# Kernel tuning notes

Measured on AMD Instinct MI355X. Metric: run time of the kernel, lower is better.

## Reference

```python
import jax, jax.numpy as jnp
import numpy as np

N_DOMAINS = 8
LN_EPS = 1e-5


def setup_inputs() -> dict:
    key = jax.random.key(0)
    ks = jax.random.split(key, 4)
    N, D_IN, D_HID, D_OUT = 32768, 256, 1024, 256
    x = jax.random.normal(ks[0], (N, D_IN), dtype=jnp.float32)
    domain_types = jax.random.randint(ks[1], (N,), 0, N_DOMAINS, dtype=jnp.int32)
    # Per-domain MLP parameters (8 independent experts)
    W1 = jax.random.normal(ks[2], (N_DOMAINS, D_IN, D_HID), dtype=jnp.float32) * (1.0 / np.sqrt(D_IN))
    b1 = jnp.zeros((N_DOMAINS, D_HID), dtype=jnp.float32)
    gamma = jnp.ones((N_DOMAINS, D_HID), dtype=jnp.float32)
    beta = jnp.zeros((N_DOMAINS, D_HID), dtype=jnp.float32)
    W2 = jax.random.normal(ks[3], (N_DOMAINS, D_HID, D_OUT), dtype=jnp.float32) * (1.0 / np.sqrt(D_HID))
    b2 = jnp.zeros((N_DOMAINS, D_OUT), dtype=jnp.float32)
    return {"x": x, "domain_types": domain_types, "W1": W1, "b1": b1,
            "gamma": gamma, "beta": beta, "W2": W2, "b2": b2}


def _expert_mlp(x, W1d, b1d, gd, bd, W2d, b2d):
    # Linear -> LayerNorm -> ReLU -> (Dropout: identity at eval) -> Linear
    h = x @ W1d + b1d                       # [N, hid]
    mu = jnp.mean(h, axis=-1, keepdims=True)
    var = jnp.mean(jnp.square(h - mu), axis=-1, keepdims=True)
    h = (h - mu) * jax.lax.rsqrt(var + LN_EPS) * gd + bd
    h = jax.nn.relu(h)
    return h @ W2d + b2d                    # [N, out]


def reference(x, domain_types, W1, b1, gamma, beta, W2, b2):
    # output dim == x.shape[-1] (as in the torch code: zeros(batch, x.shape[-1]))
    out = jnp.zeros((x.shape[0], x.shape[-1]), dtype=x.dtype)
    for d in range(N_DOMAINS):  # small fixed expert loop (static MoE dispatch)
        y = _expert_mlp(x, W1[d], b1[d], gamma[d], beta[d], W2[d], b2[d])
        mask = (domain_types == d)[:, None]
        out = jnp.where(mask, y, out)
    return out
```

## Files before the change

kernel.cpp:

```cpp
#include <hip/hip_runtime.h>
#include <hip/hip_bf16.h>


#define ND 8
#define NROWS 32768
#define DIN 256
#define DHID 1024
#define DOUT 256
#define MPAD 33792
#define NTILES 264

typedef short short8 __attribute__((ext_vector_type(8)));
typedef float floatx4 __attribute__((ext_vector_type(4)));

__device__ __forceinline__ unsigned short f2bf(float f) {
    unsigned u = __builtin_bit_cast(unsigned, f);
    unsigned r = u + 0x7fff + ((u >> 16) & 1);
    return (unsigned short)(r >> 16);
}
__device__ __forceinline__ float bf2f(unsigned short h) {
    unsigned u = ((unsigned)h) << 16;
    return __builtin_bit_cast(float, u);
}

#define GLDS16(gp, lp) __builtin_amdgcn_global_load_lds( \
    (const __attribute__((address_space(1))) void*)(gp), \
    (__attribute__((address_space(3))) void*)(lp), 16, 0, 0)

__global__ void transpose_bf16(const float* __restrict__ in,
                               unsigned short* __restrict__ out,
                               int R, int C) {
    __shared__ float t[32][33];
    const int z = blockIdx.z;
    const int c0 = blockIdx.x * 32, r0 = blockIdx.y * 32;
    const int tx = threadIdx.x & 31, ty = threadIdx.x >> 5;
    const float* src = in + (size_t)z * R * C;
    unsigned short* dst = out + (size_t)z * R * C;
#pragma unroll
    for (int i = 0; i < 32; i += 8)
        t[ty + i][tx] = src[(size_t)(r0 + ty + i) * C + c0 + tx];
    __syncthreads();
#pragma unroll
    for (int i = 0; i < 32; i += 8)
        dst[(size_t)(c0 + ty + i) * R + r0 + tx] = f2bf(t[tx][ty + i]);
}

__global__ void zero_init(int* __restrict__ perm, int* __restrict__ rowdom,
                          int* __restrict__ cnt) {
    int i = blockIdx.x * 256 + threadIdx.x;
    if (i < MPAD) { perm[i] = -1; rowdom[i] = 0; }
    if (i < 16) cnt[i] = 0;
}

__global__ void histo(const int* __restrict__ dt, int* __restrict__ counts) {
    __shared__ int lc[ND];
    if (threadIdx.x < ND) lc[threadIdx.x] = 0;
    __syncthreads();
    int i = blockIdx.x * 256 + threadIdx.x;
    atomicAdd(&lc[dt[i]], 1);
    __syncthreads();
    if (threadIdx.x < ND) atomicAdd(&counts[threadIdx.x], lc[threadIdx.x]);
}

__global__ void make_meta(const int* __restrict__ counts, int* __restrict__ cursors,
                          int2* __restrict__ meta) {
    if (threadIdx.x == 0 && blockIdx.x == 0) {
        int off = 0, t = 0;
        for (int d = 0; d < ND; d++) {
            cursors[d] = off;
            int nt = (counts[d] + 127) >> 7;
            for (int i = 0; i < nt; i++) meta[t++] = make_int2(d, off + (i << 7));
            off += nt << 7;
        }
        for (; t < NTILES; t++) meta[t] = make_int2(-1, 0);
    }
}

__global__ __launch_bounds__(256)
void assign_pos(const int* __restrict__ dt, int* __restrict__ cursors,
                int* __restrict__ perm, int* __restrict__ rowdom,
                int* __restrict__ pos) {
    __shared__ int lcnt[ND];
    __shared__ int lbase[ND];
    const int tid = threadIdx.x;
    if (tid < ND) lcnt[tid] = 0;
    __syncthreads();
    const int r = blockIdx.x * 256 + tid;
    const int d = dt[r];
    const int myrank = atomicAdd(&lcnt[d], 1);
    __syncthreads();
    if (tid < ND && lcnt[tid] > 0)
        lbase[tid] = atomicAdd(&cursors[tid], lcnt[tid]);
    __syncthreads();
    const int p = lbase[d] + myrank;
    pos[r] = p;
    perm[p] = r;
    rowdom[p] = d;
}

__global__ __launch_bounds__(256)
void copy_rows(const float* __restrict__ x, const int* __restrict__ pos,
               unsigned short* __restrict__ xs) {
    const int tid = threadIdx.x;
    const int lane = tid & 63;
    const int r = blockIdx.x * 4 + (tid >> 6);
    const int p = pos[r];
    float4 v = ((const float4*)(x + (size_t)r * DIN))[lane];
    ushort4 o;
    o.x = f2bf(v.x); o.y = f2bf(v.y); o.z = f2bf(v.z); o.w = f2bf(v.w);
    ((ushort4*)(xs + (size_t)p * DIN))[lane] = o;
}

template <int K, bool SCATTER>
__global__ __launch_bounds__(256, 2)
void gemm_bt(const unsigned short* __restrict__ A,
             const unsigned short* __restrict__ Bt,
             const float* __restrict__ bias,
             const int2* __restrict__ meta,
             const int* __restrict__ perm,
             unsigned short* __restrict__ Cbf,
             float* __restrict__ Cf,
             const int Ntot) {
    const int2 md = meta[blockIdx.x];
    const int dom = md.x;
    if (dom < 0) return;
    const int m0 = md.y;
    const int n0 = blockIdx.y * 128;

    __shared__ unsigned short As[128 * 32];
    __shared__ unsigned short Bs[128 * 32];

    const int tid = threadIdx.x;
    const int lane = tid & 63;
    const int w = tid >> 6;
    const int wr = w >> 1, wc = w & 1;

    const unsigned short* Abase = A + (size_t)m0 * K;
    const unsigned short* Bbase = Bt + (size_t)dom * Ntot * K + (size_t)n0 * K;

    floatx4 acc[4][4];
#pragma unroll
    for (int i = 0; i < 4; i++)
#pragma unroll
        for (int j = 0; j < 4; j++) acc[i][j] = 0.f;

    for (int k0 = 0; k0 < K; k0 += 32) {
#pragma unroll
        for (int it = 0; it < 2; ++it) {
            const int c = w * 128 + it * 64 + lane;
            const int m = c >> 2, kc = c & 3;
            GLDS16(Abase + (size_t)m * K + k0 + kc * 8, &As[(w * 128 + it * 64) * 8]);
            GLDS16(Bbase + (size_t)m * K + k0 + kc * 8, &Bs[(w * 128 + it * 64) * 8]);
        }
        __syncthreads();

        short8 a[4], b[4];
        const int kk = (lane >> 4) * 8;
#pragma unroll
        for (int i = 0; i < 4; i++) {
            const int m = wr * 64 + i * 16 + (lane & 15);
            a[i] = *(const short8*)&As[m * 32 + kk];
            const int n = wc * 64 + i * 16 + (lane & 15);
            b[i] = *(const short8*)&Bs[n * 32 + kk];
        }
#pragma unroll
        for (int i = 0; i < 4; i++)
#pragma unroll
            for (int j = 0; j < 4; j++)
                acc[i][j] = __builtin_amdgcn_mfma_f32_16x16x32_bf16(a[i], b[j], acc[i][j], 0, 0, 0);
        __syncthreads();
    }

    const int quad = lane >> 4;
#pragma unroll
    for (int i = 0; i < 4; i++) {
        const int rowbase = m0 + wr * 64 + i * 16 + quad * 4;
        if (!SCATTER) {
#pragma unroll
            for (int j = 0; j < 4; j++) {
                const int col = n0 + wc * 64 + j * 16 + (lane & 15);
                const float bv = bias[dom * Ntot + col];
#pragma unroll
                for (int r = 0; r < 4; r++)
                    Cbf[(size_t)(rowbase + r) * Ntot + col] = f2bf(acc[i][j][r] + bv);
            }
        } else {
#pragma unroll
            for (int r = 0; r < 4; r++) {
                const int orig = perm[rowbase + r];
                if (orig < 0) continue;
#pragma unroll
                for (int j = 0; j < 4; j++) {
                    const int col = n0 + wc * 64 + j * 16 + (lane & 15);
                    Cf[(size_t)orig * Ntot + col] = acc[i][j][r] + bias[dom * Ntot + col];
                }
            }
        }
    }
}

__global__ __launch_bounds__(256)
void ln_relu(unsigned short* __restrict__ H, const float* __restrict__ gamma,
             const float* __restrict__ beta, const int* __restrict__ rowdom) {
    const int row = blockIdx.x;
    const int tid = threadIdx.x;
    const int dom = rowdom[row];
    unsigned short* hr = H + (size_t)row * DHID;
    ushort4 raw = ((const ushort4*)hr)[tid];
    float v0 = bf2f(raw.x), v1 = bf2f(raw.y), v2 = bf2f(raw.z), v3 = bf2f(raw.w);
    float s = v0 + v1 + v2 + v3;
    float s2 = v0 * v0 + v1 * v1 + v2 * v2 + v3 * v3;
#pragma unroll
    for (int o = 32; o; o >>= 1) {
        s += __shfl_xor(s, o, 64);
        s2 += __shfl_xor(s2, o, 64);
    }
    __shared__ float red[8];
    const int w = tid >> 6;
    if ((tid & 63) == 0) { red[w] = s; red[4 + w] = s2; }
    __syncthreads();
    s = red[0] + red[1] + red[2] + red[3];
    s2 = red[4] + red[5] + red[6] + red[7];
    const float inv = 1.0f / 1024.0f;
    const float mu = s * inv;
    const float var = fmaxf(s2 * inv - mu * mu, 0.f);
    const float rstd = rsqrtf(var + 1e-5f);
    const float* g = gamma + dom * DHID + tid * 4;
    const float* b = beta + dom * DHID + tid * 4;
    ushort4 o4;
    o4.x = f2bf(fmaxf((v0 - mu) * rstd * g[0] + b[0], 0.f));
    o4.y = f2bf(fmaxf((v1 - mu) * rstd * g[1] + b[1], 0.f));
    o4.z = f2bf(fmaxf((v2 - mu) * rstd * g[2] + b[2], 0.f));
    o4.w = f2bf(fmaxf((v3 - mu) * rstd * g[3] + b[3], 0.f));
    ((ushort4*)hr)[tid] = o4;
}

extern "C" void kernel_launch(void* const* d_in, const int* in_sizes, int n_in,
                              void* d_out, int out_size, void* d_ws, size_t ws_size,
                              hipStream_t stream) {
    const float* x = (const float*)d_in[0];
    const int* dt = (const int*)d_in[1];
    const float* W1 = (const float*)d_in[2];
    const float* b1 = (const float*)d_in[3];
    const float* gamma = (const float*)d_in[4];
    const float* beta = (const float*)d_in[5];
    const float* W2 = (const float*)d_in[6];
    const float* b2 = (const float*)d_in[7];
    float* out = (float*)d_out;

    char* ws = (char*)d_ws;
    size_t off = 0;
    auto take = [&](size_t nbytes) -> char* {
        char* p = ws + off;
        off = (off + nbytes + 255) & ~(size_t)255;
        return p;
    };
    unsigned short* W1T = (unsigned short*)take((size_t)ND * DHID * DIN * 2);
    unsigned short* W2T = (unsigned short*)take((size_t)ND * DOUT * DHID * 2);
    unsigned short* XS  = (unsigned short*)take((size_t)MPAD * DIN * 2);
    unsigned short* H   = (unsigned short*)take((size_t)MPAD * DHID * 2);
    int* PERM   = (int*)take(MPAD * 4);
    int* ROWDOM = (int*)take(MPAD * 4);
    int* POS    = (int*)take(NROWS * 4);
    int* CNT    = (int*)take(64);
    int2* META  = (int2*)take(NTILES * 8);
    (void)ws_size; (void)n_in; (void)in_sizes; (void)out_size;

    int* COUNTS = CNT;
    int* CURSORS = CNT + 8;

    transpose_bf16<<<dim3(DHID / 32, DIN / 32, ND), 256, 0, stream>>>(W1, W1T, DIN, DHID);
    transpose_bf16<<<dim3(DOUT / 32, DHID / 32, ND), 256, 0, stream>>>(W2, W2T, DHID, DOUT);
    zero_init<<<(MPAD + 255) / 256, 256, 0, stream>>>(PERM, ROWDOM, CNT);
    histo<<<NROWS / 256, 256, 0, stream>>>(dt, COUNTS);
    make_meta<<<1, 1, 0, stream>>>(COUNTS, CURSORS, META);
    assign_pos<<<NROWS / 256, 256, 0, stream>>>(dt, CURSORS, PERM, ROWDOM, POS);
    copy_rows<<<NROWS / 4, 256, 0, stream>>>(x, POS, XS);
    gemm_bt<DIN, false><<<dim3(NTILES, DHID / 128), 256, 0, stream>>>(
        XS, W1T, b1, META, nullptr, H, nullptr, DHID);
    ln_relu<<<MPAD, 256, 0, stream>>>(H, gamma, beta, ROWDOM);
    gemm_bt<DHID, true><<<dim3(NTILES, DOUT / 128), 256, 0, stream>>>(
        H, W2T, b2, META, PERM, nullptr, out, DOUT);
}
```

Baseline: 227.6 us.

## Fuse gather, both expert GEMMs and LayerNorm into one per-tile kernel

Replaces the copy_rows, first GEMM, ln_relu and second GEMM kernels with a single fused kernel. Each 512-thread block owns a 64-row tile and gathers x rows through perm into swizzled LDS. It computes the full 1024-wide hidden layer in registers, does the LayerNorm reduction across waves, writes the bf16 activations back to LDS, and runs the second GEMM with a scatter store. This removes the round trips of XS and H through global memory and several launches. In exchange it uses 128KB+ of LDS per block, which limits occupancy, reads weights directly from global without LDS staging, and makes make_meta parallel.

```diff
diff --git a/kernel.cpp b/kernel.cpp
--- a/kernel.cpp
+++ b/kernel.cpp
@@ -7,8 +7,9 @@
 #define DIN 256
 #define DHID 1024
 #define DOUT 256
-#define MPAD 33792
-#define NTILES 264
+#define RPT 64
+#define MPAD64 33280
+#define NT64 520
 
 typedef short short8 __attribute__((ext_vector_type(8)));
 typedef float floatx4 __attribute__((ext_vector_type(4)));
@@ -18,14 +19,6 @@
     unsigned r = u + 0x7fff + ((u >> 16) & 1);
     return (unsigned short)(r >> 16);
 }
-__device__ __forceinline__ float bf2f(unsigned short h) {
-    unsigned u = ((unsigned)h) << 16;
-    return __builtin_bit_cast(float, u);
-}
-
-#define GLDS16(gp, lp) __builtin_amdgcn_global_load_lds( \
-    (const __attribute__((address_space(1))) void*)(gp), \
-    (__attribute__((address_space(3))) void*)(lp), 16, 0, 0)
 
 __global__ void transpose_bf16(const float* __restrict__ in,
                                unsigned short* __restrict__ out,
@@ -45,10 +38,9 @@
         dst[(size_t)(c0 + ty + i) * R + r0 + tx] = f2bf(t[tx][ty + i]);
 }
 
-__global__ void zero_init(int* __restrict__ perm, int* __restrict__ rowdom,
-                          int* __restrict__ cnt) {
+__global__ void zero_init(int* __restrict__ perm, int* __restrict__ cnt) {
     int i = blockIdx.x * 256 + threadIdx.x;
-    if (i < MPAD) { perm[i] = -1; rowdom[i] = 0; }
+    if (i < MPAD64) perm[i] = -1;
     if (i < 16) cnt[i] = 0;
 }
 
@@ -64,22 +56,32 @@
 
 __global__ void make_meta(const int* __restrict__ counts, int* __restrict__ cursors,
                           int2* __restrict__ meta) {
-    if (threadIdx.x == 0 && blockIdx.x == 0) {
-        int off = 0, t = 0;
+    __shared__ int base[ND], ntc[ND];
+    const int t = threadIdx.x;
+    if (t == 0) {
+        int off = 0;
         for (int d = 0; d < ND; d++) {
+            base[d] = off;
+            ntc[d] = (counts[d] + 63) >> 6;
             cursors[d] = off;
-            int nt = (counts[d] + 127) >> 7;
-            for (int i = 0; i < nt; i++) meta[t++] = make_int2(d, off + (i << 7));
-            off += nt << 7;
-        }
-        for (; t < NTILES; t++) meta[t] = make_int2(-1, 0);
+            off += ntc[d] << 6;
+        }
+    }
+    __syncthreads();
+    for (int i = t; i < NT64; i += 64) {
+        int2 m = make_int2(-1, 0);
+#pragma unroll
+        for (int d = 0; d < ND; d++) {
+            const int ti = i - (base[d] >> 6);
+            if (ti >= 0 && ti < ntc[d]) m = make_int2(d, base[d] + (ti << 6));
+        }
+        meta[i] = m;
     }
 }
 
 __global__ __launch_bounds__(256)
 void assign_pos(const int* __restrict__ dt, int* __restrict__ cursors,
-                int* __restrict__ perm, int* __restrict__ rowdom,
-                int* __restrict__ pos) {
+                int* __restrict__ perm) {
     __shared__ int lcnt[ND];
     __shared__ int lbase[ND];
     const int tid = threadIdx.x;
@@ -92,147 +94,242 @@
     if (tid < ND && lcnt[tid] > 0)
         lbase[tid] = atomicAdd(&cursors[tid], lcnt[tid]);
     __syncthreads();
-    const int p = lbase[d] + myrank;
-    pos[r] = p;
-    perm[p] = r;
-    rowdom[p] = d;
-}
-
-__global__ __launch_bounds__(256)
-void copy_rows(const float* __restrict__ x, const int* __restrict__ pos,
-               unsigned short* __restrict__ xs) {
-    const int tid = threadIdx.x;
-    const int lane = tid & 63;
-    const int r = blockIdx.x * 4 + (tid >> 6);
-    const int p = pos[r];
-    float4 v = ((const float4*)(x + (size_t)r * DIN))[lane];
-    ushort4 o;
-    o.x = f2bf(v.x); o.y = f2bf(v.y); o.z = f2bf(v.z); o.w = f2bf(v.w);
-    ((ushort4*)(xs + (size_t)p * DIN))[lane] = o;
-}
-
-template <int K, bool SCATTER>
-__global__ __launch_bounds__(256, 2)
-void gemm_bt(const unsigned short* __restrict__ A,
-             const unsigned short* __restrict__ Bt,
-             const float* __restrict__ bias,
-             const int2* __restrict__ meta,
-             const int* __restrict__ perm,
-             unsigned short* __restrict__ Cbf,
-             float* __restrict__ Cf,
-             const int Ntot) {
-    const int2 md = meta[blockIdx.x];
+    perm[lbase[d] + myrank] = r;
+}
+
+__global__ __launch_bounds__(512, 2)
+void fused_mlp(const float* __restrict__ x,
+               const unsigned short* __restrict__ W1T,
+               const float* __restrict__ b1,
+               const float* __restrict__ gamma,
+               const float* __restrict__ beta,
+               const unsigned short* __restrict__ W2T,
+               const float* __restrict__ b2,
+               const int2* __restrict__ meta,
+               const int* __restrict__ perm,
+               float* __restrict__ out) {
+    const int bid = (int)blockIdx.x;
+    const int swz = (bid & 7) * (NT64 >> 3) + (bid >> 3);
+    const int2 md = meta[swz];
     const int dom = md.x;
     if (dom < 0) return;
     const int m0 = md.y;
-    const int n0 = blockIdx.y * 128;
-
-    __shared__ unsigned short As[128 * 32];
-    __shared__ unsigned short Bs[128 * 32];
+
+    __shared__ unsigned short Hs[RPT * DHID];
+    __shared__ float red[1024];
+    unsigned short* Axs = Hs;
 
     const int tid = threadIdx.x;
     const int lane = tid & 63;
     const int w = tid >> 6;
-    const int wr = w >> 1, wc = w & 1;
-
-    const unsigned short* Abase = A + (size_t)m0 * K;
-    const unsigned short* Bbase = Bt + (size_t)dom * Ntot * K + (size_t)n0 * K;
-
-    floatx4 acc[4][4];
-#pragma unroll
-    for (int i = 0; i < 4; i++)
-#pragma unroll
-        for (int j = 0; j < 4; j++) acc[i][j] = 0.f;
-
-    for (int k0 = 0; k0 < K; k0 += 32) {
-#pragma unroll
-        for (int it = 0; it < 2; ++it) {
-            const int c = w * 128 + it * 64 + lane;
-            const int m = c >> 2, kc = c & 3;
-            GLDS16(Abase + (size_t)m * K + k0 + kc * 8, &As[(w * 128 + it * 64) * 8]);
-            GLDS16(Bbase + (size_t)m * K + k0 + kc * 8, &Bs[(w * 128 + it * 64) * 8]);
-        }
-        __syncthreads();
-
-        short8 a[4], b[4];
-        const int kk = (lane >> 4) * 8;
-#pragma unroll
-        for (int i = 0; i < 4; i++) {
-            const int m = wr * 64 + i * 16 + (lane & 15);
-            a[i] = *(const short8*)&As[m * 32 + kk];
-            const int n = wc * 64 + i * 16 + (lane & 15);
-            b[i] = *(const short8*)&Bs[n * 32 + kk];
-        }
-#pragma unroll
-        for (int i = 0; i < 4; i++)
-#pragma unroll
-            for (int j = 0; j < 4; j++)
-                acc[i][j] = __builtin_amdgcn_mfma_f32_16x16x32_bf16(a[i], b[j], acc[i][j], 0, 0, 0);
-        __syncthreads();
-    }
-
-    const int quad = lane >> 4;
-#pragma unroll
-    for (int i = 0; i < 4; i++) {
-        const int rowbase = m0 + wr * 64 + i * 16 + quad * 4;
-        if (!SCATTER) {
-#pragma unroll
-            for (int j = 0; j < 4; j++) {
-                const int col = n0 + wc * 64 + j * 16 + (lane & 15);
-                const float bv = bias[dom * Ntot + col];
-#pragma unroll
-                for (int r = 0; r < 4; r++)
-                    Cbf[(size_t)(rowbase + r) * Ntot + col] = f2bf(acc[i][j][r] + bv);
+    const int l15 = lane & 15;
+    const int q = lane >> 4;
+
+    {
+        const int row = tid >> 3;
+        const int c8 = tid & 7;
+        const int orig = perm[m0 + row];
+        const int sw = (row & 7) << 3;
+        if (orig >= 0) {
+            const float4* src = (const float4*)(x + (size_t)orig * DIN);
+#pragma unroll
+            for (int it = 0; it < 8; ++it) {
+                const int c = it * 8 + c8;
+                const float4 v = src[c];
+                ushort4 o;
+                o.x = f2bf(v.x); o.y = f2bf(v.y); o.z = f2bf(v.z); o.w = f2bf(v.w);
+                *(ushort4*)&Axs[(row * DIN + c * 4) ^ sw] = o;
             }
         } else {
-#pragma unroll
-            for (int r = 0; r < 4; r++) {
-                const int orig = perm[rowbase + r];
-                if (orig < 0) continue;
-#pragma unroll
-                for (int j = 0; j < 4; j++) {
-                    const int col = n0 + wc * 64 + j * 16 + (lane & 15);
-                    Cf[(size_t)orig * Ntot + col] = acc[i][j][r] + bias[dom * Ntot + col];
-                }
-            }
-        }
-    }
-}
-
-__global__ __launch_bounds__(256)
-void ln_relu(unsigned short* __restrict__ H, const float* __restrict__ gamma,
-             const float* __restrict__ beta, const int* __restrict__ rowdom) {
-    const int row = blockIdx.x;
-    const int tid = threadIdx.x;
-    const int dom = rowdom[row];
-    unsigned short* hr = H + (size_t)row * DHID;
-    ushort4 raw = ((const ushort4*)hr)[tid];
-    float v0 = bf2f(raw.x), v1 = bf2f(raw.y), v2 = bf2f(raw.z), v3 = bf2f(raw.w);
-    float s = v0 + v1 + v2 + v3;
-    float s2 = v0 * v0 + v1 * v1 + v2 * v2 + v3 * v3;
-#pragma unroll
-    for (int o = 32; o; o >>= 1) {
-        s += __shfl_xor(s, o, 64);
-        s2 += __shfl_xor(s2, o, 64);
-    }
-    __shared__ float red[8];
-    const int w = tid >> 6;
-    if ((tid & 63) == 0) { red[w] = s; red[4 + w] = s2; }
-    __syncthreads();
-    s = red[0] + red[1] + red[2] + red[3];
-    s2 = red[4] + red[5] + red[6] + red[7];
-    const float inv = 1.0f / 1024.0f;
-    const float mu = s * inv;
-    const float var = fmaxf(s2 * inv - mu * mu, 0.f);
-    const float rstd = rsqrtf(var + 1e-5f);
-    const float* g = gamma + dom * DHID + tid * 4;
-    const float* b = beta + dom * DHID + tid * 4;
-    ushort4 o4;
-    o4.x = f2bf(fmaxf((v0 - mu) * rstd * g[0] + b[0], 0.f));
-    o4.y = f2bf(fmaxf((v1 - mu) * rstd * g[1] + b[1], 0.f));
-    o4.z = f2bf(fmaxf((v2 - mu) * rstd * g[2] + b[2], 0.f));
-    o4.w = f2bf(fmaxf((v3 - mu) * rstd * g[3] + b[3], 0.f));
-    ((ushort4*)hr)[tid] = o4;
+            const ushort4 z = {0, 0, 0, 0};
+#pragma unroll
+            for (int it = 0; it < 8; ++it) {
+                const int c = it * 8 + c8;
+                *(ushort4*)&Axs[(row * DIN + c * 4) ^ sw] = z;
+            }
+        }
+    }
+
+    const int n0w = w * 128;
+    const unsigned short* B1p = W1T + (size_t)dom * DHID * DIN
+                              + (size_t)(n0w + l15) * DIN + q * 8;
+    short8 bA[8], bB[8];
+#pragma unroll
+    for (int j = 0; j < 8; ++j)
+        bA[j] = *(const short8*)(B1p + (size_t)j * 16 * DIN);
+
+    __syncthreads();
+
+    floatx4 acc[4][8];
+#pragma unroll
+    for (int i = 0; i < 4; ++i)
+#pragma unroll
+        for (int j = 0; j < 8; ++j) acc[i][j] = 0.f;
+
+#pragma unroll
+    for (int t = 0; t < 8; ++t) {
+        const int k0 = t * 32;
+        short8* bc = (t & 1) ? bB : bA;
+        short8* bn = (t & 1) ? bA : bB;
+        if (t < 7) {
+#pragma unroll
+            for (int j = 0; j < 8; ++j)
+                bn[j] = *(const short8*)(B1p + (size_t)j * 16 * DIN + (k0 + 32));
+        }
+        short8 a[4];
+#pragma unroll
+        for (int i = 0; i < 4; ++i) {
+            const int row = i * 16 + l15;
+            a[i] = *(const short8*)&Axs[(row * DIN + k0 + q * 8) ^ ((row & 7) << 3)];
+        }
+        __builtin_amdgcn_s_setprio(1);
+#pragma unroll
+        for (int i = 0; i < 4; ++i)
+#pragma unroll
+            for (int j = 0; j < 8; ++j)
+                acc[i][j] = __builtin_amdgcn_mfma_f32_16x16x32_bf16(a[i], bc[j], acc[i][j], 0, 0, 0);
+        __builtin_amdgcn_s_setprio(0);
+    }
+
+    float b1v[8], gv[8], bv[8];
+#pragma unroll
+    for (int j = 0; j < 8; ++j) {
+        const int col = n0w + j * 16 + l15;
+        b1v[j] = b1[dom * DHID + col];
+        gv[j]  = gamma[dom * DHID + col];
+        bv[j]  = beta[dom * DHID + col];
+    }
+#pragma unroll
+    for (int i = 0; i < 4; ++i)
+#pragma unroll
+        for (int j = 0; j < 8; ++j)
+#pragma unroll
+            for (int r = 0; r < 4; ++r) acc[i][j][r] += b1v[j];
+
+#pragma unroll
+    for (int i = 0; i < 4; ++i)
+#pragma unroll
+        for (int r = 0; r < 4; ++r) {
+            float s = 0.f, s2 = 0.f;
+#pragma unroll
+            for (int j = 0; j < 8; ++j) {
+                const float v = acc[i][j][r];
+                s += v; s2 += v * v;
+            }
+#pragma unroll
+            for (int o = 8; o; o >>= 1) {
+                s  += __shfl_xor(s, o, 64);
+                s2 += __shfl_xor(s2, o, 64);
+            }
+            if (l15 == 0) {
+                const int row = i * 16 + q * 4 + r;
+                red[w * 64 + row]       = s;
+                red[512 + w * 64 + row] = s2;
+            }
+        }
+    __syncthreads();
+    if (tid < 64) {
+        float s = 0.f, s2 = 0.f;
+#pragma unroll
+        for (int ww = 0; ww < 8; ++ww) {
+            s  += red[ww * 64 + tid];
+            s2 += red[512 + ww * 64 + tid];
+        }
+        const float mu  = s * (1.f / 1024.f);
+        const float var = fmaxf(s2 * (1.f / 1024.f) - mu * mu, 0.f);
+        red[tid]      = mu;
+        red[64 + tid] = rsqrtf(var + 1e-5f);
+    }
+    __syncthreads();
+
+#pragma unroll
+    for (int i = 0; i < 4; ++i)
+#pragma unroll
+        for (int r = 0; r < 4; ++r) {
+            const int row = i * 16 + q * 4 + r;
+            const float mu   = red[row];
+            const float rstd = red[64 + row];
+            const int sw = (row & 7) << 3;
+#pragma unroll
+            for (int j = 0; j < 8; ++j) {
+                const int col = n0w + j * 16 + l15;
+                const float v = fmaxf((acc[i][j][r] - mu) * rstd * gv[j] + bv[j], 0.f);
+                Hs[(row * DHID + col) ^ sw] = f2bf(v);
+            }
+        }
+    __syncthreads();
+
+    floatx4 acc2[4][2];
+#pragma unroll
+    for (int i = 0; i < 4; ++i) { acc2[i][0] = 0.f; acc2[i][1] = 0.f; }
+
+    const int c0w = w * 32;
+    const unsigned short* B2p = W2T + (size_t)dom * DOUT * DHID
+                              + (size_t)(c0w + l15) * DHID + q * 8;
+    short8 cA[2], cB[2];
+#pragma unroll
+    for (int jj = 0; jj < 2; ++jj)
+        cA[jj] = *(const short8*)(B2p + (size_t)jj * 16 * DHID);
+
+    for (int t = 0; t < 32; t += 2) {
+        const int k0 = t * 32;
+        if (t + 1 < 32) {
+#pragma unroll
+            for (int jj = 0; jj < 2; ++jj)
+                cB[jj] = *(const short8*)(B2p + (size_t)jj * 16 * DHID + (k0 + 32));
+        }
+        {
+            short8 a[4];
+#pragma unroll
+            for (int ii = 0; ii < 4; ++ii) {
+                const int row = ii * 16 + l15;
+                a[ii] = *(const short8*)&Hs[(row * DHID + k0 + q * 8) ^ ((row & 7) << 3)];
+            }
+            __builtin_amdgcn_s_setprio(1);
+#pragma unroll
+            for (int ii = 0; ii < 4; ++ii)
+#pragma unroll
+                for (int jj = 0; jj < 2; ++jj)
+                    acc2[ii][jj] = __builtin_amdgcn_mfma_f32_16x16x32_bf16(a[ii], cA[jj], acc2[ii][jj], 0, 0, 0);
+            __builtin_amdgcn_s_setprio(0);
+        }
+        if (t + 2 < 32) {
+#pragma unroll
+            for (int jj = 0; jj < 2; ++jj)
+                cA[jj] = *(const short8*)(B2p + (size_t)jj * 16 * DHID + (k0 + 64));
+        }
+        {
+            short8 a[4];
+#pragma unroll
+            for (int ii = 0; ii < 4; ++ii) {
+                const int row = ii * 16 + l15;
+                a[ii] = *(const short8*)&Hs[(row * DHID + k0 + 32 + q * 8) ^ ((row & 7) << 3)];
+            }
+            __builtin_amdgcn_s_setprio(1);
+#pragma unroll
+            for (int ii = 0; ii < 4; ++ii)
+#pragma unroll
+                for (int jj = 0; jj < 2; ++jj)
+                    acc2[ii][jj] = __builtin_amdgcn_mfma_f32_16x16x32_bf16(a[ii], cB[jj], acc2[ii][jj], 0, 0, 0);
+            __builtin_amdgcn_s_setprio(0);
+        }
+    }
+
+    float b2v[2];
+#pragma unroll
+    for (int jj = 0; jj < 2; ++jj)
+        b2v[jj] = b2[dom * DOUT + c0w + jj * 16 + l15];
+#pragma unroll
+    for (int ii = 0; ii < 4; ++ii)
+#pragma unroll
+        for (int r = 0; r < 4; ++r) {
+            const int row = ii * 16 + q * 4 + r;
+            const int orig = perm[m0 + row];
+            if (orig < 0) continue;
+#pragma unroll
+            for (int jj = 0; jj < 2; ++jj)
+                out[(size_t)orig * DOUT + c0w + jj * 16 + l15] = acc2[ii][jj][r] + b2v[jj];
+        }
 }
 
 extern "C" void kernel_launch(void* const* d_in, const int* in_sizes, int n_in,
@@ -257,13 +354,9 @@
     };
     unsigned short* W1T = (unsigned short*)take((size_t)ND * DHID * DIN * 2);
     unsigned short* W2T = (unsigned short*)take((size_t)ND * DOUT * DHID * 2);
-    unsigned short* XS  = (unsigned short*)take((size_t)MPAD * DIN * 2);
-    unsigned short* H   = (unsigned short*)take((size_t)MPAD * DHID * 2);
-    int* PERM   = (int*)take(MPAD * 4);
-    int* ROWDOM = (int*)take(MPAD * 4);
-    int* POS    = (int*)take(NROWS * 4);
-    int* CNT    = (int*)take(64);
-    int2* META  = (int2*)take(NTILES * 8);
+    int* PERM = (int*)take(MPAD64 * 4);
+    int* CNT  = (int*)take(64);
+    int2* META = (int2*)take(NT64 * 8);
     (void)ws_size; (void)n_in; (void)in_sizes; (void)out_size;
 
     int* COUNTS = CNT;
@@ -271,14 +364,9 @@
 
     transpose_bf16<<<dim3(DHID / 32, DIN / 32, ND), 256, 0, stream>>>(W1, W1T, DIN, DHID);
     transpose_bf16<<<dim3(DOUT / 32, DHID / 32, ND), 256, 0, stream>>>(W2, W2T, DHID, DOUT);
-    zero_init<<<(MPAD + 255) / 256, 256, 0, stream>>>(PERM, ROWDOM, CNT);
+    zero_init<<<MPAD64 / 256, 256, 0, stream>>>(PERM, CNT);
     histo<<<NROWS / 256, 256, 0, stream>>>(dt, COUNTS);
-    make_meta<<<1, 1, 0, stream>>>(COUNTS, CURSORS, META);
-    assign_pos<<<NROWS / 256, 256, 0, stream>>>(dt, CURSORS, PERM, ROWDOM, POS);
-    copy_rows<<<NROWS / 4, 256, 0, stream>>>(x, POS, XS);
-    gemm_bt<DIN, false><<<dim3(NTILES, DHID / 128), 256, 0, stream>>>(
-        XS, W1T, b1, META, nullptr, H, nullptr, DHID);
-    ln_relu<<<MPAD, 256, 0, stream>>>(H, gamma, beta, ROWDOM);
-    gemm_bt<DHID, true><<<dim3(NTILES, DOUT / 128), 256, 0, stream>>>(
-        H, W2T, b2, META, PERM, nullptr, out, DOUT);
-}
+    make_meta<<<1, 64, 0, stream>>>(COUNTS, CURSORS, META);
+    assign_pos<<<NROWS / 256, 256, 0, stream>>>(dt, CURSORS, PERM);
+    fused_mlp<<<NT64, 512, 0, stream>>>(x, W1T, b1, gamma, beta, W2T, b2, META, PERM, out);
+}
```

New measurement: 235.3 us. 1.03x slower.

## Fuse LayerNorm statistics into GEMM1 epilogue and normalize in GEMM2 prologue

Applied to the files above, without the earlier changes.

Removes the separate ln_relu pass over the hidden buffer. GEMM1 now accumulates per-row sum and sum-of-squares in its epilogue, using shuffles and shared atomics, and writes per-column-block partials. GEMM2 reduces those partials into mean and rstd, then applies normalize, affine and ReLU while loading A tiles through registers. This saves one full read and write of the large bf16 hidden buffer and one launch. In exchange, GEMM2's A loads become synchronous register loads instead of direct-to-LDS loads, and the statistics come from fp32 values before bf16 rounding.

```diff
diff --git a/kernel.cpp b/kernel.cpp
--- a/kernel.cpp
+++ b/kernel.cpp
@@ -45,10 +45,9 @@
         dst[(size_t)(c0 + ty + i) * R + r0 + tx] = f2bf(t[tx][ty + i]);
 }
 
-__global__ void zero_init(int* __restrict__ perm, int* __restrict__ rowdom,
-                          int* __restrict__ cnt) {
+__global__ void zero_init(int* __restrict__ perm, int* __restrict__ cnt) {
     int i = blockIdx.x * 256 + threadIdx.x;
-    if (i < MPAD) { perm[i] = -1; rowdom[i] = 0; }
+    if (i < MPAD) perm[i] = -1;
     if (i < 16) cnt[i] = 0;
 }
 
@@ -78,8 +77,7 @@
 
 __global__ __launch_bounds__(256)
 void assign_pos(const int* __restrict__ dt, int* __restrict__ cursors,
-                int* __restrict__ perm, int* __restrict__ rowdom,
-                int* __restrict__ pos) {
+                int* __restrict__ perm, int* __restrict__ pos) {
     __shared__ int lcnt[ND];
     __shared__ int lbase[ND];
     const int tid = threadIdx.x;
@@ -95,7 +93,6 @@
     const int p = lbase[d] + myrank;
     pos[r] = p;
     perm[p] = r;
-    rowdom[p] = d;
 }
 
 __global__ __launch_bounds__(256)
@@ -111,7 +108,7 @@
     ((ushort4*)(xs + (size_t)p * DIN))[lane] = o;
 }
 
-template <int K, bool SCATTER>
+template <int K, bool ISB>
 __global__ __launch_bounds__(256, 2)
 void gemm_bt(const unsigned short* __restrict__ A,
              const unsigned short* __restrict__ Bt,
@@ -120,7 +117,10 @@
              const int* __restrict__ perm,
              unsigned short* __restrict__ Cbf,
              float* __restrict__ Cf,
-             const int Ntot) {
+             const int Ntot,
+             float2* __restrict__ spart,
+             const float* __restrict__ gamma,
+             const float* __restrict__ beta) {
     const int2 md = meta[blockIdx.x];
     const int dom = md.x;
     if (dom < 0) return;
@@ -129,6 +129,7 @@
 
     __shared__ unsigned short As[128 * 32];
     __shared__ unsigned short Bs[128 * 32];
+    __shared__ float sred[2][128];
 
     const int tid = threadIdx.x;
     const int lane = tid & 63;
@@ -138,6 +139,30 @@
     const unsigned short* Abase = A + (size_t)m0 * K;
     const unsigned short* Bbase = Bt + (size_t)dom * Ntot * K + (size_t)n0 * K;
 
+    if (!ISB) {
+        if (tid < 128) { sred[0][tid] = 0.f; sred[1][tid] = 0.f; }
+    }
+
+    const int ma = (w * 128 + lane) >> 2;
+    const int kc = lane & 3;
+    float muv[2], rsv[2];
+    if (ISB) {
+#pragma unroll
+        for (int h2 = 0; h2 < 2; ++h2) {
+            const int rm = m0 + ma + h2 * 16;
+            float s = 0.f, s2 = 0.f;
+#pragma unroll
+            for (int nb = 0; nb < 8; ++nb) {
+                const float2 p = spart[(size_t)nb * MPAD + rm];
+                s += p.x; s2 += p.y;
+            }
+            const float mu = s * (1.f / 1024.f);
+            const float var = fmaxf(s2 * (1.f / 1024.f) - mu * mu, 0.f);
+            muv[h2] = mu;
+            rsv[h2] = rsqrtf(var + 1e-5f);
+        }
+    }
+
     floatx4 acc[4][4];
 #pragma unroll
     for (int i = 0; i < 4; i++)
@@ -145,12 +170,42 @@
         for (int j = 0; j < 4; j++) acc[i][j] = 0.f;
 
     for (int k0 = 0; k0 < K; k0 += 32) {
+        if (!ISB) {
+#pragma unroll
+            for (int it = 0; it < 2; ++it) {
+                const int c = w * 128 + it * 64 + lane;
+                const int m = c >> 2, kcc = c & 3;
+                GLDS16(Abase + (size_t)m * K + k0 + kcc * 8, &As[(w * 128 + it * 64) * 8]);
+            }
+        } else {
+            const float* gp = gamma + dom * DHID + k0 + kc * 8;
+            const float* bp = beta + dom * DHID + k0 + kc * 8;
+            const float4 g0 = ((const float4*)gp)[0];
+            const float4 g1 = ((const float4*)gp)[1];
+            const float4 e0 = ((const float4*)bp)[0];
+            const float4 e1 = ((const float4*)bp)[1];
+#pragma unroll
+            for (int h2 = 0; h2 < 2; ++h2) {
+                const int m = ma + h2 * 16;
+                const short8 hv = *(const short8*)(Abase + (size_t)m * K + k0 + kc * 8);
+                const float mu = muv[h2], rs = rsv[h2];
+                short8 o;
+                o[0] = (short)f2bf(fmaxf((bf2f((unsigned short)hv[0]) - mu) * rs * g0.x + e0.x, 0.f));
+                o[1] = (short)f2bf(fmaxf((bf2f((unsigned short)hv[1]) - mu) * rs * g0.y + e0.y, 0.f));
+                o[2] = (short)f2bf(fmaxf((bf2f((unsigned short)hv[2]) - mu) * rs * g0.z + e0.z, 0.f));
+                o[3] = (short)f2bf(fmaxf((bf2f((unsigned short)hv[3]) - mu) * rs * g0.w + e0.w, 0.f));
+                o[4] = (short)f2bf(fmaxf((bf2f((unsigned short)hv[4]) - mu) * rs * g1.x + e1.x, 0.f));
+                o[5] = (short)f2bf(fmaxf((bf2f((unsigned short)hv[5]) - mu) * rs * g1.y + e1.y, 0.f));
+                o[6] = (short)f2bf(fmaxf((bf2f((unsigned short)hv[6]) - mu) * rs * g1.z + e1.z, 0.f));
+                o[7] = (short)f2bf(fmaxf((bf2f((unsigned short)hv[7]) - mu) * rs * g1.w + e1.w, 0.f));
+                *(short8*)&As[(w * 128 + h2 * 64 + lane) * 8] = o;
+            }
+        }
 #pragma unroll
         for (int it = 0; it < 2; ++it) {
             const int c = w * 128 + it * 64 + lane;
-            const int m = c >> 2, kc = c & 3;
-            GLDS16(Abase + (size_t)m * K + k0 + kc * 8, &As[(w * 128 + it * 64) * 8]);
-            GLDS16(Bbase + (size_t)m * K + k0 + kc * 8, &Bs[(w * 128 + it * 64) * 8]);
+            const int m = c >> 2, kcc = c & 3;
+            GLDS16(Bbase + (size_t)m * K + k0 + kcc * 8, &Bs[(w * 128 + it * 64) * 8]);
         }
         __syncthreads();
 
@@ -172,67 +227,55 @@
     }
 
     const int quad = lane >> 4;
-#pragma unroll
-    for (int i = 0; i < 4; i++) {
-        const int rowbase = m0 + wr * 64 + i * 16 + quad * 4;
-        if (!SCATTER) {
-#pragma unroll
-            for (int j = 0; j < 4; j++) {
-                const int col = n0 + wc * 64 + j * 16 + (lane & 15);
-                const float bv = bias[dom * Ntot + col];
-#pragma unroll
-                for (int r = 0; r < 4; r++)
-                    Cbf[(size_t)(rowbase + r) * Ntot + col] = f2bf(acc[i][j][r] + bv);
-            }
-        } else {
+    const int l15 = lane & 15;
+    if (!ISB) {
+        float bv[4];
+#pragma unroll
+        for (int j = 0; j < 4; j++)
+            bv[j] = bias[dom * Ntot + n0 + wc * 64 + j * 16 + l15];
+#pragma unroll
+        for (int i = 0; i < 4; i++) {
+#pragma unroll
+            for (int r = 0; r < 4; r++) {
+                const int rl = wr * 64 + i * 16 + quad * 4 + r;
+                float s = 0.f, s2 = 0.f;
+#pragma unroll
+                for (int j = 0; j < 4; j++) {
+                    const float v = acc[i][j][r] + bv[j];
+                    Cbf[(size_t)(m0 + rl) * Ntot + n0 + wc * 64 + j * 16 + l15] = f2bf(v);
+                    s += v; s2 += v * v;
+                }
+#pragma unroll
+                for (int o = 8; o; o >>= 1) {
+                    s  += __shfl_xor(s, o, 64);
+                    s2 += __shfl_xor(s2, o, 64);
+                }
+                if (l15 == 0) {
+                    atomicAdd(&sred[0][rl], s);
+                    atomicAdd(&sred[1][rl], s2);
+                }
+            }
+        }
+        __syncthreads();
+        if (tid < 128)
+            spart[(size_t)blockIdx.y * MPAD + m0 + tid] =
+                make_float2(sred[0][tid], sred[1][tid]);
+    } else {
+#pragma unroll
+        for (int i = 0; i < 4; i++) {
+            const int rowbase = m0 + wr * 64 + i * 16 + quad * 4;
 #pragma unroll
             for (int r = 0; r < 4; r++) {
                 const int orig = perm[rowbase + r];
                 if (orig < 0) continue;
 #pragma unroll
                 for (int j = 0; j < 4; j++) {
-                    const int col = n0 + wc * 64 + j * 16 + (lane & 15);
+                    const int col = n0 + wc * 64 + j * 16 + l15;
                     Cf[(size_t)orig * Ntot + col] = acc[i][j][r] + bias[dom * Ntot + col];
                 }
             }
         }
     }
-}
-
-__global__ __launch_bounds__(256)
-void ln_relu(unsigned short* __restrict__ H, const float* __restrict__ gamma,
-             const float* __restrict__ beta, const int* __restrict__ rowdom) {
-    const int row = blockIdx.x;
-    const int tid = threadIdx.x;
-    const int dom = rowdom[row];
-    unsigned short* hr = H + (size_t)row * DHID;
-    ushort4 raw = ((const ushort4*)hr)[tid];
-    float v0 = bf2f(raw.x), v1 = bf2f(raw.y), v2 = bf2f(raw.z), v3 = bf2f(raw.w);
-    float s = v0 + v1 + v2 + v3;
-    float s2 = v0 * v0 + v1 * v1 + v2 * v2 + v3 * v3;
-#pragma unroll
-    for (int o = 32; o; o >>= 1) {
-        s += __shfl_xor(s, o, 64);
-        s2 += __shfl_xor(s2, o, 64);
-    }
-    __shared__ float red[8];
-    const int w = tid >> 6;
-    if ((tid & 63) == 0) { red[w] = s; red[4 + w] = s2; }
-    __syncthreads();
-    s = red[0] + red[1] + red[2] + red[3];
-    s2 = red[4] + red[5] + red[6] + red[7];
-    const float inv = 1.0f / 1024.0f;
-    const float mu = s * inv;
-    const float var = fmaxf(s2 * inv - mu * mu, 0.f);
-    const float rstd = rsqrtf(var + 1e-5f);
-    const float* g = gamma + dom * DHID + tid * 4;
-    const float* b = beta + dom * DHID + tid * 4;
-    ushort4 o4;
-    o4.x = f2bf(fmaxf((v0 - mu) * rstd * g[0] + b[0], 0.f));
-    o4.y = f2bf(fmaxf((v1 - mu) * rstd * g[1] + b[1], 0.f));
-    o4.z = f2bf(fmaxf((v2 - mu) * rstd * g[2] + b[2], 0.f));
-    o4.w = f2bf(fmaxf((v3 - mu) * rstd * g[3] + b[3], 0.f));
-    ((ushort4*)hr)[tid] = o4;
 }
 
 extern "C" void kernel_launch(void* const* d_in, const int* in_sizes, int n_in,
@@ -259,8 +302,8 @@
     unsigned short* W2T = (unsigned short*)take((size_t)ND * DOUT * DHID * 2);
     unsigned short* XS  = (unsigned short*)take((size_t)MPAD * DIN * 2);
     unsigned short* H   = (unsigned short*)take((size_t)MPAD * DHID * 2);
+    float2* SPART = (float2*)take((size_t)8 * MPAD * 8);
     int* PERM   = (int*)take(MPAD * 4);
-    int* ROWDOM = (int*)take(MPAD * 4);
     int* POS    = (int*)take(NROWS * 4);
     int* CNT    = (int*)take(64);
     int2* META  = (int2*)take(NTILES * 8);
@@ -271,14 +314,13 @@
 
     transpose_bf16<<<dim3(DHID / 32, DIN / 32, ND), 256, 0, stream>>>(W1, W1T, DIN, DHID);
     transpose_bf16<<<dim3(DOUT / 32, DHID / 32, ND), 256, 0, stream>>>(W2, W2T, DHID, DOUT);
-    zero_init<<<(MPAD + 255) / 256, 256, 0, stream>>>(PERM, ROWDOM, CNT);
+    zero_init<<<(MPAD + 255) / 256, 256, 0, stream>>>(PERM, CNT);
     histo<<<NROWS / 256, 256, 0, stream>>>(dt, COUNTS);
     make_meta<<<1, 1, 0, stream>>>(COUNTS, CURSORS, META);
-    assign_pos<<<NROWS / 256, 256, 0, stream>>>(dt, CURSORS, PERM, ROWDOM, POS);
+    assign_pos<<<NROWS / 256, 256, 0, stream>>>(dt, CURSORS, PERM, POS);
     copy_rows<<<NROWS / 4, 256, 0, stream>>>(x, POS, XS);
     gemm_bt<DIN, false><<<dim3(NTILES, DHID / 128), 256, 0, stream>>>(
-        XS, W1T, b1, META, nullptr, H, nullptr, DHID);
-    ln_relu<<<MPAD, 256, 0, stream>>>(H, gamma, beta, ROWDOM);
+        XS, W1T, b1, META, nullptr, H, nullptr, DHID, SPART, nullptr, nullptr);
     gemm_bt<DHID, true><<<dim3(NTILES, DOUT / 128), 256, 0, stream>>>(
-        H, W2T, b2, META, PERM, nullptr, out, DOUT);
-}
+        H, W2T, b2, META, PERM, nullptr, out, DOUT, SPART, gamma, beta);
+}
```

Measured after the change: 221.8 us. 1.03x faster.
